# Optimization experiments

Measured on AMD Instinct MI355X. Metric: run time of the kernel, lower is better.

## Reference

```python
import jax, jax.numpy as jnp
import numpy as np
import math

DIM = 1024
NUM_HEADS = 16
HEAD_DIM = DIM // NUM_HEADS
BLOCK_SIZE = 64


def _block_mask(src_blocks, tgt_blocks, num_blocks):
    # Block-level BigBird mask: global first/last block columns, sliding window of 1, random blocks.
    i = jnp.arange(num_blocks)[:, None]
    j = jnp.arange(num_blocks)[None, :]
    band = jnp.abs(i - j) <= 1
    glob = (j == 0) | (j == num_blocks - 1)
    bm = band | glob
    bm = bm.at[src_blocks, tgt_blocks].set(True)
    return bm  # [nb, nb] bool


def setup_inputs() -> dict:
    key = jax.random.key(0)
    ks = jax.random.split(key, 12)
    B, S = 2, 2048
    x = jax.random.normal(ks[0], (B, S, DIM), dtype=jnp.float32)
    scale = 0.02
    Wq = jax.random.normal(ks[1], (DIM, DIM), dtype=jnp.float32) * scale
    bq = jnp.zeros((DIM,), dtype=jnp.float32)
    Wk = jax.random.normal(ks[2], (DIM, DIM), dtype=jnp.float32) * scale
    bk = jnp.zeros((DIM,), dtype=jnp.float32)
    Wv = jax.random.normal(ks[3], (DIM, DIM), dtype=jnp.float32) * scale
    bv = jnp.zeros((DIM,), dtype=jnp.float32)
    Wo = jax.random.normal(ks[4], (DIM, DIM), dtype=jnp.float32) * scale
    bo = jnp.zeros((DIM,), dtype=jnp.float32)
    num_blocks = S // BLOCK_SIZE
    src_blocks = jax.random.randint(ks[5], (3,), 0, num_blocks, dtype=jnp.int32)
    tgt_blocks = jax.random.randint(ks[6], (3,), 0, num_blocks, dtype=jnp.int32)
    return {"x": x, "Wq": Wq, "bq": bq, "Wk": Wk, "bk": bk, "Wv": Wv, "bv": bv,
            "Wo": Wo, "bo": bo, "src_blocks": src_blocks, "tgt_blocks": tgt_blocks}


def reference(x, Wq, bq, Wk, bk, Wv, bv, Wo, bo, src_blocks, tgt_blocks):
    B, S, _ = x.shape
    nb = S // BLOCK_SIZE
    # NOTE: original torch code uses .view (not transpose) to split heads; replicate faithfully.
    q = (x @ Wq.T + bq).reshape(B, NUM_HEADS, S, HEAD_DIM)
    k = (x @ Wk.T + bk).reshape(B, NUM_HEADS, S, HEAD_DIM)
    v = (x @ Wv.T + bv).reshape(B, NUM_HEADS, S, HEAD_DIM)
    bm = _block_mask(src_blocks, tgt_blocks, nb)
    mask = jnp.repeat(jnp.repeat(bm, BLOCK_SIZE, axis=0), BLOCK_SIZE, axis=1)  # [S, S]
    scores = jnp.einsum('bhqd,bhkd->bhqk', q, k) / math.sqrt(HEAD_DIM)
    scores = jnp.where(mask[None, None], scores, jnp.float32(-1e9))
    attn = jax.nn.softmax(scores, axis=-1)
    out = jnp.einsum('bhqk,bhkd->bhqd', attn, v)
    out = out.transpose(0, 2, 1, 3).reshape(B, S, DIM)
    return out @ Wo.T + bo
```

## Files before the change

### kernel.cpp

```cpp
#include <hip/hip_runtime.h>
#include <math.h>

typedef __attribute__((ext_vector_type(8))) short short8;
typedef __attribute__((ext_vector_type(4))) float f32x4;

#define SEQ 2048
#define NB  32

__device__ __forceinline__ unsigned short f2bf(float f) {
    unsigned u = __float_as_uint(f);
    u = (u + 0x7FFFu + ((u >> 16) & 1u)) >> 16;
    return (unsigned short)u;
}

__device__ __forceinline__ void gload16(const unsigned short* g, unsigned short* l) {
    __builtin_amdgcn_global_load_lds(
        (__attribute__((address_space(1))) void*)(void*)(g),
        (__attribute__((address_space(3))) void*)(l), 16, 0, 0);
}

__global__ __launch_bounds__(256) void cvt_all(const float* __restrict__ x,
                                               const float* __restrict__ w0,
                                               const float* __restrict__ w1,
                                               const float* __restrict__ w2,
                                               const float* __restrict__ w3,
                                               unsigned short* __restrict__ ox,
                                               unsigned short* __restrict__ o0,
                                               unsigned short* __restrict__ o1,
                                               unsigned short* __restrict__ o2,
                                               unsigned short* __restrict__ o3) {
    const int which = blockIdx.y;
    const float* in = (which == 0) ? x : (which == 1) ? w0 : (which == 2) ? w1
                       : (which == 3) ? w2 : w3;
    unsigned short* out = (which == 0) ? ox : (which == 1) ? o0 : (which == 2) ? o1
                          : (which == 3) ? o2 : o3;
    const int n8 = (which == 0) ? 524288 : 131072;
    int i = blockIdx.x * 256 + threadIdx.x;
    const int stride = gridDim.x * 256;
    for (; i < n8; i += stride) {
        const float4 a = ((const float4*)in)[i * 2];
        const float4 b = ((const float4*)in)[i * 2 + 1];
        uint4 o;
        o.x = f2bf(a.x) | ((unsigned)f2bf(a.y) << 16);
        o.y = f2bf(a.z) | ((unsigned)f2bf(a.w) << 16);
        o.z = f2bf(b.x) | ((unsigned)f2bf(b.y) << 16);
        o.w = f2bf(b.z) | ((unsigned)f2bf(b.w) << 16);
        ((uint4*)out)[i] = o;
    }
}

template <int BF16OUT, int BN>
__global__ __launch_bounds__(256) void gemm_bt(const unsigned short* __restrict__ A,
                                               const unsigned short* __restrict__ Wall,
                                               const float* __restrict__ b0,
                                               const float* __restrict__ b1,
                                               const float* __restrict__ b2,
                                               unsigned short* __restrict__ outb,
                                               float* __restrict__ outf) {
    constexpr int MI = (BN == 128) ? 4 : 2;
    constexpr int NI = 4;
    __shared__ __align__(16) unsigned short SMEM[2 * 128 * 32 + 2 * BN * 32];
    unsigned short* As0 = SMEM;
    unsigned short* As1 = SMEM + 128 * 32;
    unsigned short* Bs0 = SMEM + 2 * 128 * 32;
    unsigned short* Bs1 = SMEM + 2 * 128 * 32 + BN * 32;

    const int t = threadIdx.x;
    const int w = t >> 6, l = t & 63;
    const int bx = blockIdx.x;
    const int which = (BN == 128) ? (bx >> 3) : 0;
    const int n0 = (BN == 128) ? (bx & 7) * 128 : bx * 64;
    const int m0 = blockIdx.y * 128;
    const unsigned short* W = Wall + (size_t)which * (1024ull * 1024);
    const float* bias = (which == 0) ? b0 : (which == 1) ? b1 : b2;

    const int wr = (BN == 128) ? (w >> 1) * 64 : w * 32;
    const int wc = (BN == 128) ? (w & 1) * 64 : 0;

    f32x4 acc[MI][NI];
#pragma unroll
    for (int i = 0; i < MI; ++i)
#pragma unroll
        for (int j = 0; j < NI; ++j) acc[i][j] = f32x4{0.f, 0.f, 0.f, 0.f};

    const unsigned short* Ag = A + (size_t)(m0 + w * 32 + (l >> 2)) * 1024 + (l & 3) * 8;
    const unsigned short* Wg =
        W + (size_t)(n0 + ((BN == 128) ? w * 32 : w * 16) + (l >> 2)) * 1024 + (l & 3) * 8;

    auto STAGE = [&](unsigned short* Asb, unsigned short* Bsb, int k0) {
        gload16(Ag + k0, Asb + w * 1024);
        gload16(Ag + k0 + 16 * 1024, Asb + w * 1024 + 512);
        gload16(Wg + k0, Bsb + ((BN == 128) ? w * 1024 : w * 512));
        if (BN == 128) gload16(Wg + k0 + 16 * 1024, Bsb + w * 1024 + 512);
    };
    auto COMPUTE = [&](const unsigned short* Asb, const unsigned short* Bsb) {
        short8 af[MI], bfr[NI];
#pragma unroll
        for (int mi = 0; mi < MI; ++mi)
            af[mi] = *(const short8*)&Asb[(wr + mi * 16 + (l & 15)) * 32 + (l >> 4) * 8];
#pragma unroll
        for (int ni = 0; ni < NI; ++ni)
            bfr[ni] = *(const short8*)&Bsb[(wc + ni * 16 + (l & 15)) * 32 + (l >> 4) * 8];
#pragma unroll
        for (int mi = 0; mi < MI; ++mi)
#pragma unroll
            for (int ni = 0; ni < NI; ++ni)
                acc[mi][ni] = __builtin_amdgcn_mfma_f32_16x16x32_bf16(af[mi], bfr[ni],
                                                                      acc[mi][ni], 0, 0, 0);
    };
#define WAITV_INFLIGHT()                                                  \
    do {                                                                  \
        if constexpr (BN == 128)                                          \
            asm volatile("s_waitcnt vmcnt(4)" ::: "memory");              \
        else                                                              \
            asm volatile("s_waitcnt vmcnt(3)" ::: "memory");              \
        __builtin_amdgcn_sched_barrier(0);                                \
    } while (0)
#define BAR()                                                             \
    do {                                                                  \
        __builtin_amdgcn_s_barrier();                                     \
        __builtin_amdgcn_sched_barrier(0);                                \
    } while (0)
#define READS_DONE_BAR()                                                  \
    do {                                                                  \
        asm volatile("s_waitcnt lgkmcnt(0)" ::: "memory");                \
        __builtin_amdgcn_sched_barrier(0);                                \
        __builtin_amdgcn_s_barrier();                                     \
        __builtin_amdgcn_sched_barrier(0);                                \
    } while (0)

    STAGE(As0, Bs0, 0);
#pragma unroll 1
    for (int kt2 = 0; kt2 < 16; ++kt2) {
        STAGE(As1, Bs1, (kt2 * 2 + 1) * 32);
        WAITV_INFLIGHT();
        BAR();
        COMPUTE(As0, Bs0);
        READS_DONE_BAR();

        if (kt2 < 15) {
            STAGE(As0, Bs0, (kt2 * 2 + 2) * 32);
            WAITV_INFLIGHT();
        } else {
            asm volatile("s_waitcnt vmcnt(0)" ::: "memory");
            __builtin_amdgcn_sched_barrier(0);
        }
        BAR();
        COMPUTE(As1, Bs1);
        if (kt2 < 15) READS_DONE_BAR();
    }
#undef WAITV_INFLIGHT
#undef BAR
#undef READS_DONE_BAR

    __syncthreads();
    const int g = l >> 4, c = l & 15;
    if constexpr (BF16OUT) {
        unsigned short* eb = SMEM + w * (32 * 72);
        unsigned short* outw = outb + (size_t)which * (4096ull * 1024);
        const int r1 = l >> 1, hh = (l & 1) * 32;
#pragma unroll
        for (int half = 0; half < 2; ++half) {
#pragma unroll
            for (int ni = 0; ni < NI; ++ni) {
                const float bv = bias[n0 + wc + ni * 16 + c];
#pragma unroll
                for (int mi2 = 0; mi2 < 2; ++mi2)
#pragma unroll
                    for (int j = 0; j < 4; ++j)
                        eb[(mi2 * 16 + g * 4 + j) * 72 + ni * 16 + c] =
                            f2bf(acc[half * 2 + mi2][ni][j] + bv);
            }
            asm volatile("s_waitcnt lgkmcnt(0)" ::: "memory");
            __builtin_amdgcn_sched_barrier(0);
            const unsigned short* src = eb + r1 * 72 + hh;
            unsigned short* dst =
                &outw[(size_t)(m0 + wr + half * 32 + r1) * 1024 + n0 + wc + hh];
#pragma unroll
            for (int q = 0; q < 4; ++q)
                *(uint4*)(dst + q * 8) = *(const uint4*)(src + q * 8);
            asm volatile("s_waitcnt lgkmcnt(0)" ::: "memory");
            __builtin_amdgcn_sched_barrier(0);
        }
    } else {
        float* ef = (float*)SMEM + w * (16 * 68);
        const int r2 = l >> 2, qq = (l & 3) * 16;
#pragma unroll
        for (int mi = 0; mi < MI; ++mi) {
#pragma unroll
            for (int ni = 0; ni < NI; ++ni) {
                const float bv = bias[n0 + wc + ni * 16 + c];
#pragma unroll
                for (int j = 0; j < 4; ++j)
                    ef[(g * 4 + j) * 68 + ni * 16 + c] = acc[mi][ni][j] + bv;
            }
            asm volatile("s_waitcnt lgkmcnt(0)" ::: "memory");
            __builtin_amdgcn_sched_barrier(0);
            const float* srcf = ef + r2 * 68 + qq;
            float* dstf = &outf[(size_t)(m0 + wr + mi * 16 + r2) * 1024 + n0 + wc + qq];
#pragma unroll
            for (int q = 0; q < 4; ++q)
                *(float4*)(dstf + q * 4) = *(const float4*)(srcf + q * 4);
            asm volatile("s_waitcnt lgkmcnt(0)" ::: "memory");
            __builtin_amdgcn_sched_barrier(0);
        }
    }
}

__global__ __launch_bounds__(256) void gemm_obt(const unsigned short* __restrict__ A,
                                                const unsigned short* __restrict__ W,
                                                const float* __restrict__ bias,
                                                float* __restrict__ outf) {
    constexpr int MI = 2, NI = 4;
    __shared__ __align__(16) unsigned short SMEM[2 * (128 + 64) * 64];
    unsigned short* As0 = SMEM;
    unsigned short* As1 = SMEM + 128 * 64;
    unsigned short* Bs0 = SMEM + 2 * 128 * 64;
    unsigned short* Bs1 = SMEM + 2 * 128 * 64 + 64 * 64;

    const int t = threadIdx.x;
    const int w = t >> 6, l = t & 63;
    const int n0 = blockIdx.x * 64;
    const int m0 = blockIdx.y * 128;

    const int wr = w * 32, wc = 0;

    f32x4 acc[MI][NI];
#pragma unroll
    for (int i = 0; i < MI; ++i)
#pragma unroll
        for (int j = 0; j < NI; ++j) acc[i][j] = f32x4{0.f, 0.f, 0.f, 0.f};

    const int scol = ((l & 7) ^ (l >> 3)) * 8;
    const unsigned short* Ag = A + (size_t)(m0 + w * 32 + (l >> 3)) * 1024 + scol;
    const unsigned short* Wg = W + (size_t)(n0 + w * 16 + (l >> 3)) * 1024 + scol;

    auto STAGE = [&](unsigned short* Asb, unsigned short* Bsb, int k0) {
        gload16(Ag + k0, Asb + (w * 32) * 64);
        gload16(Ag + k0 + 8 * 1024, Asb + (w * 32 + 8) * 64);
        gload16(Ag + k0 + 16 * 1024, Asb + (w * 32 + 16) * 64);
        gload16(Ag + k0 + 24 * 1024, Asb + (w * 32 + 24) * 64);
        gload16(Wg + k0, Bsb + (w * 16) * 64);
        gload16(Wg + k0 + 8 * 1024, Bsb + (w * 16 + 8) * 64);
    };
    auto COMPUTE = [&](const unsigned short* Asb, const unsigned short* Bsb) {
#pragma unroll
        for (int kk = 0; kk < 2; ++kk) {
            short8 af[MI], bfr[NI];
#pragma unroll
            for (int mi = 0; mi < MI; ++mi) {
                const int r = wr + mi * 16 + (l & 15);
                const int slot = (kk * 4 + (l >> 4)) ^ (r & 7);
                af[mi] = *(const short8*)&Asb[r * 64 + slot * 8];
            }
#pragma unroll
            for (int ni = 0; ni < NI; ++ni) {
                const int r = wc + ni * 16 + (l & 15);
                const int slot = (kk * 4 + (l >> 4)) ^ (r & 7);
                bfr[ni] = *(const short8*)&Bsb[r * 64 + slot * 8];
            }
#pragma unroll
            for (int mi = 0; mi < MI; ++mi)
#pragma unroll
                for (int ni = 0; ni < NI; ++ni)
                    acc[mi][ni] = __builtin_amdgcn_mfma_f32_16x16x32_bf16(
                        af[mi], bfr[ni], acc[mi][ni], 0, 0, 0);
        }
    };
#define WV6()                                                             \
    do {                                                                  \
        asm volatile("s_waitcnt vmcnt(6)" ::: "memory");                  \
        __builtin_amdgcn_sched_barrier(0);                                \
    } while (0)
#define BAR()                                                             \
    do {                                                                  \
        __builtin_amdgcn_s_barrier();                                     \
        __builtin_amdgcn_sched_barrier(0);                                \
    } while (0)
#define READS_DONE_BAR()                                                  \
    do {                                                                  \
        asm volatile("s_waitcnt lgkmcnt(0)" ::: "memory");                \
        __builtin_amdgcn_sched_barrier(0);                                \
        __builtin_amdgcn_s_barrier();                                     \
        __builtin_amdgcn_sched_barrier(0);                                \
    } while (0)

    STAGE(As0, Bs0, 0);
#pragma unroll 1
    for (int kt2 = 0; kt2 < 8; ++kt2) {
        STAGE(As1, Bs1, (kt2 * 2 + 1) * 64);
        WV6();
        BAR();
        COMPUTE(As0, Bs0);
        READS_DONE_BAR();

        if (kt2 < 7) {
            STAGE(As0, Bs0, (kt2 * 2 + 2) * 64);
            WV6();
        } else {
            asm volatile("s_waitcnt vmcnt(0)" ::: "memory");
            __builtin_amdgcn_sched_barrier(0);
        }
        BAR();
        COMPUTE(As1, Bs1);
        if (kt2 < 7) READS_DONE_BAR();
    }
#undef WV6
#undef BAR
#undef READS_DONE_BAR

    __syncthreads();
    const int g = l >> 4, c = l & 15;
    float* ef = (float*)SMEM + w * (16 * 68);
    const int r2 = l >> 2, qq = (l & 3) * 16;
#pragma unroll
    for (int mi = 0; mi < MI; ++mi) {
#pragma unroll
        for (int ni = 0; ni < NI; ++ni) {
            const float bv = bias[n0 + wc + ni * 16 + c];
#pragma unroll
            for (int j = 0; j < 4; ++j)
                ef[(g * 4 + j) * 68 + ni * 16 + c] = acc[mi][ni][j] + bv;
        }
        asm volatile("s_waitcnt lgkmcnt(0)" ::: "memory");
        __builtin_amdgcn_sched_barrier(0);
        const float* srcf = ef + r2 * 68 + qq;
        float* dstf = &outf[(size_t)(m0 + wr + mi * 16 + r2) * 1024 + n0 + wc + qq];
#pragma unroll
        for (int q = 0; q < 4; ++q)
            *(float4*)(dstf + q * 4) = *(const float4*)(srcf + q * 4);
        asm volatile("s_waitcnt lgkmcnt(0)" ::: "memory");
        __builtin_amdgcn_sched_barrier(0);
    }
}

__global__ __launch_bounds__(256) void attn_mfma(const unsigned short* __restrict__ qb_,
                                                 const unsigned short* __restrict__ kb_,
                                                 const unsigned short* __restrict__ vb_,
                                                 const int* __restrict__ srcb,
                                                 const int* __restrict__ tgtb,
                                                 unsigned short* __restrict__ outb) {
    __shared__ __align__(16) unsigned short Ks[64 * 72];
    __shared__ __align__(16) unsigned short Vs[64 * 72];
    __shared__ __align__(16) unsigned short Ps[4][16 * 72];

    const int t = threadIdx.x, w = t >> 6, l = t & 63;
    const int qi = blockIdx.x, h = blockIdx.y, b = blockIdx.z;
    const int g = l >> 4, c = l & 15;

    unsigned mask = 1u | (1u << (NB - 1)) | (1u << qi);
    if (qi > 0) mask |= 1u << (qi - 1);
    if (qi < NB - 1) mask |= 1u << (qi + 1);
#pragma unroll
    for (int tt = 0; tt < 3; ++tt)
        if (srcb[tt] == qi) mask |= 1u << (tgtb[tt] & 31);

    const size_t ho = (size_t)(b * 16 + h) * (SEQ * 64);
    const unsigned short* Q = qb_ + ho;
    const unsigned short* K = kb_ + ho;
    const unsigned short* V = vb_ + ho;

    short8 qf[2];
    {
        const unsigned short* qrow = Q + (size_t)(qi * 64 + w * 16 + c) * 64;
        qf[0] = *(const short8*)(qrow + g * 8);
        qf[1] = *(const short8*)(qrow + 32 + g * 8);
    }

    f32x4 oacc[4];
#pragma unroll
    for (int d = 0; d < 4; ++d) oacc[d] = f32x4{0.f, 0.f, 0.f, 0.f};
    float mrun = -INFINITY, lsum = 0.f;

    const int sr = t >> 2, sc = (t & 3) * 16;

    uint4 k0, k1, v0, v1;
    {
        const unsigned short* ksrc = K + (size_t)(0 * 64 + sr) * 64 + sc;
        const unsigned short* vsrc = V + (size_t)(0 * 64 + sr) * 64 + sc;
        k0 = *(const uint4*)ksrc; k1 = *(const uint4*)(ksrc + 8);
        v0 = *(const uint4*)vsrc; v1 = *(const uint4*)(vsrc + 8);
    }

    int kb = 0;
    while (kb < NB) {
        int nxt = kb + 1;
        while (nxt < NB && !((mask >> nxt) & 1u)) ++nxt;

        __syncthreads();
        *(uint4*)&Ks[sr * 72 + sc] = k0;
        *(uint4*)&Ks[sr * 72 + sc + 8] = k1;
        {
            const unsigned short* p0 = (const unsigned short*)&v0;
            const unsigned short* p1 = (const unsigned short*)&v1;
#pragma unroll
            for (int e = 0; e < 8; ++e) {
                Vs[(sc + e) * 72 + sr] = p0[e];
                Vs[(sc + 8 + e) * 72 + sr] = p1[e];
            }
        }
        __syncthreads();

        if (nxt < NB) {
            const unsigned short* ksrc = K + (size_t)(nxt * 64 + sr) * 64 + sc;
            const unsigned short* vsrc = V + (size_t)(nxt * 64 + sr) * 64 + sc;
            k0 = *(const uint4*)ksrc; k1 = *(const uint4*)(ksrc + 8);
            v0 = *(const uint4*)vsrc; v1 = *(const uint4*)(vsrc + 8);
        }

        f32x4 sacc[4];
#pragma unroll
        for (int kt = 0; kt < 4; ++kt) sacc[kt] = f32x4{0.f, 0.f, 0.f, 0.f};
#pragma unroll
        for (int kt = 0; kt < 4; ++kt) {
#pragma unroll
            for (int ks = 0; ks < 2; ++ks) {
                const short8 ka = *(const short8*)&Ks[(kt * 16 + c) * 72 + ks * 32 + g * 8];
                sacc[kt] = __builtin_amdgcn_mfma_f32_16x16x32_bf16(ka, qf[ks], sacc[kt], 0, 0, 0);
            }
        }

        float sv[16];
        float tmax = -INFINITY;
#pragma unroll
        for (int kt = 0; kt < 4; ++kt)
#pragma unroll
            for (int j = 0; j < 4; ++j) {
                const float x = sacc[kt][j] * 0.125f;
                sv[kt * 4 + j] = x;
                tmax = fmaxf(tmax, x);
            }
        tmax = fmaxf(tmax, __shfl_xor(tmax, 16));
        tmax = fmaxf(tmax, __shfl_xor(tmax, 32));
        const float newm = fmaxf(mrun, tmax);
        const float corr = __expf(mrun - newm);
        float ps = 0.f;
#pragma unroll
        for (int e = 0; e < 16; ++e) {
            const float p = __expf(sv[e] - newm);
            sv[e] = p;
            ps += p;
        }
        ps += __shfl_xor(ps, 16);
        ps += __shfl_xor(ps, 32);
        lsum = lsum * corr + ps;
        mrun = newm;
#pragma unroll
        for (int d = 0; d < 4; ++d)
#pragma unroll
            for (int j = 0; j < 4; ++j) oacc[d][j] *= corr;

        unsigned short* pw = &Ps[w][c * 72];
#pragma unroll
        for (int kt = 0; kt < 4; ++kt) {
            uint2 pk;
            pk.x = f2bf(sv[kt * 4 + 0]) | ((unsigned)f2bf(sv[kt * 4 + 1]) << 16);
            pk.y = f2bf(sv[kt * 4 + 2]) | ((unsigned)f2bf(sv[kt * 4 + 3]) << 16);
            *(uint2*)&pw[kt * 16 + g * 4] = pk;
        }
        asm volatile("s_waitcnt lgkmcnt(0)" ::: "memory");
        __builtin_amdgcn_sched_barrier(0);

#pragma unroll
        for (int ks = 0; ks < 2; ++ks) {
            const short8 pb = *(const short8*)&Ps[w][c * 72 + ks * 32 + g * 8];
#pragma unroll
            for (int dt = 0; dt < 4; ++dt) {
                const short8 va = *(const short8*)&Vs[(dt * 16 + c) * 72 + ks * 32 + g * 8];
                oacc[dt] = __builtin_amdgcn_mfma_f32_16x16x32_bf16(va, pb, oacc[dt], 0, 0, 0);
            }
        }

        kb = nxt;
    }

    const float inv = 1.f / lsum;
    unsigned short* orow = outb + (size_t)(b * SEQ + qi * 64 + w * 16 + c) * 1024 + h * 64;
#pragma unroll
    for (int dt = 0; dt < 4; ++dt)
#pragma unroll
        for (int j = 0; j < 4; ++j)
            orow[dt * 16 + g * 4 + j] = f2bf(oacc[dt][j] * inv);
}

extern "C" void kernel_launch(void* const* d_in, const int* in_sizes, int n_in,
                              void* d_out, int out_size, void* d_ws, size_t ws_size,
                              hipStream_t stream) {
    const float* x  = (const float*)d_in[0];
    const float* Wq = (const float*)d_in[1];
    const float* bq = (const float*)d_in[2];
    const float* Wk = (const float*)d_in[3];
    const float* bk = (const float*)d_in[4];
    const float* Wv = (const float*)d_in[5];
    const float* bv = (const float*)d_in[6];
    const float* Wo = (const float*)d_in[7];
    const float* bo = (const float*)d_in[8];
    const int* srcb = (const int*)d_in[9];
    const int* tgtb = (const int*)d_in[10];

    unsigned short* wsu = (unsigned short*)d_ws;
    unsigned short* xbf   = wsu;
    unsigned short* wqkv  = wsu + 4194304ull;
    unsigned short* wobf  = wsu + 7340032ull;
    unsigned short* qkvbf = wsu + 8388608ull;
    unsigned short* attbf = wsu + 25165824ull;

    hipLaunchKernelGGL(cvt_all, dim3(512, 5), dim3(256), 0, stream,
                       x, Wq, Wk, Wv, Wo,
                       xbf, wqkv, wqkv + 1048576ull, wqkv + 2097152ull, wobf);

    hipLaunchKernelGGL((gemm_bt<1, 128>), dim3(24, 32), dim3(256), 0, stream,
                       xbf, wqkv, bq, bk, bv, qkvbf, (float*)nullptr);

    hipLaunchKernelGGL(attn_mfma, dim3(32, 16, 2), dim3(256), 0, stream,
                       qkvbf, qkvbf + 4194304ull, qkvbf + 2ull * 4194304ull,
                       srcb, tgtb, attbf);

    hipLaunchKernelGGL(gemm_obt, dim3(16, 32), dim3(256), 0, stream,
                       attbf, wobf, bo, (float*)d_out);

    (void)in_sizes; (void)n_in; (void)out_size; (void)ws_size;
}
```

Before: 92.30 us.

## Split-K the output projection GEMM with atomic accumulation

Splits the K dimension of the output projection GEMM into two halves across blockIdx.z, doubling the grid from 512 to 1024 blocks. Partial results are combined with float atomicAdd into the output, which is zeroed by a memset beforehand, and only the first split adds the bias. The aim is better CU occupancy for this small GEMM. In exchange it adds scattered uncoalesced atomic traffic, an extra memset, and non-deterministic summation order.

```diff
diff --git a/kernel.cpp b/kernel.cpp
--- a/kernel.cpp
+++ b/kernel.cpp
@@ -207,10 +207,10 @@
     }
 }
 
-__global__ __launch_bounds__(256) void gemm_obt(const unsigned short* __restrict__ A,
-                                                const unsigned short* __restrict__ W,
-                                                const float* __restrict__ bias,
-                                                float* __restrict__ outf) {
+__global__ __launch_bounds__(256) void gemm_obt_sk(const unsigned short* __restrict__ A,
+                                                   const unsigned short* __restrict__ W,
+                                                   const float* __restrict__ bias,
+                                                   float* __restrict__ outf) {
     constexpr int MI = 2, NI = 4;
     __shared__ __align__(16) unsigned short SMEM[2 * (128 + 64) * 64];
     unsigned short* As0 = SMEM;
@@ -222,6 +222,8 @@
     const int w = t >> 6, l = t & 63;
     const int n0 = blockIdx.x * 64;
     const int m0 = blockIdx.y * 128;
+    const int kz = blockIdx.z;
+    const int kbase = kz * 512;
 
     const int wr = w * 32, wc = 0;
 
@@ -285,17 +287,17 @@
         __builtin_amdgcn_sched_barrier(0);                                \
     } while (0)
 
-    STAGE(As0, Bs0, 0);
+    STAGE(As0, Bs0, kbase);
 #pragma unroll 1
-    for (int kt2 = 0; kt2 < 8; ++kt2) {
-        STAGE(As1, Bs1, (kt2 * 2 + 1) * 64);
+    for (int kt2 = 0; kt2 < 4; ++kt2) {
+        STAGE(As1, Bs1, kbase + (kt2 * 2 + 1) * 64);
         WV6();
         BAR();
         COMPUTE(As0, Bs0);
         READS_DONE_BAR();
 
-        if (kt2 < 7) {
-            STAGE(As0, Bs0, (kt2 * 2 + 2) * 64);
+        if (kt2 < 3) {
+            STAGE(As0, Bs0, kbase + (kt2 * 2 + 2) * 64);
             WV6();
         } else {
             asm volatile("s_waitcnt vmcnt(0)" ::: "memory");
@@ -303,34 +305,24 @@
         }
         BAR();
         COMPUTE(As1, Bs1);
-        if (kt2 < 7) READS_DONE_BAR();
+        if (kt2 < 3) READS_DONE_BAR();
     }
 #undef WV6
 #undef BAR
 #undef READS_DONE_BAR
 
-    __syncthreads();
     const int g = l >> 4, c = l & 15;
-    float* ef = (float*)SMEM + w * (16 * 68);
-    const int r2 = l >> 2, qq = (l & 3) * 16;
-#pragma unroll
-    for (int mi = 0; mi < MI; ++mi) {
-#pragma unroll
-        for (int ni = 0; ni < NI; ++ni) {
-            const float bv = bias[n0 + wc + ni * 16 + c];
-#pragma unroll
-            for (int j = 0; j < 4; ++j)
-                ef[(g * 4 + j) * 68 + ni * 16 + c] = acc[mi][ni][j] + bv;
-        }
-        asm volatile("s_waitcnt lgkmcnt(0)" ::: "memory");
-        __builtin_amdgcn_sched_barrier(0);
-        const float* srcf = ef + r2 * 68 + qq;
-        float* dstf = &outf[(size_t)(m0 + wr + mi * 16 + r2) * 1024 + n0 + wc + qq];
-#pragma unroll
-        for (int q = 0; q < 4; ++q)
-            *(float4*)(dstf + q * 4) = *(const float4*)(srcf + q * 4);
-        asm volatile("s_waitcnt lgkmcnt(0)" ::: "memory");
-        __builtin_amdgcn_sched_barrier(0);
+#pragma unroll
+    for (int ni = 0; ni < NI; ++ni) {
+        const int n = n0 + wc + ni * 16 + c;
+        const float bv = (kz == 0) ? bias[n] : 0.f;
+#pragma unroll
+        for (int mi = 0; mi < MI; ++mi)
+#pragma unroll
+            for (int j = 0; j < 4; ++j) {
+                const size_t m = (size_t)(m0 + wr + mi * 16 + g * 4 + j);
+                atomicAdd(&outf[m * 1024 + n], acc[mi][ni][j] + bv);
+            }
     }
 }
 
@@ -505,6 +497,8 @@
     unsigned short* qkvbf = wsu + 8388608ull;
     unsigned short* attbf = wsu + 25165824ull;
 
+    hipMemsetAsync(d_out, 0, (size_t)out_size * sizeof(float), stream);
+
     hipLaunchKernelGGL(cvt_all, dim3(512, 5), dim3(256), 0, stream,
                        x, Wq, Wk, Wv, Wo,
                        xbf, wqkv, wqkv + 1048576ull, wqkv + 2097152ull, wobf);
@@ -516,7 +510,7 @@
                        qkvbf, qkvbf + 4194304ull, qkvbf + 2ull * 4194304ull,
                        srcb, tgtb, attbf);
 
-    hipLaunchKernelGGL(gemm_obt, dim3(16, 32), dim3(256), 0, stream,
+    hipLaunchKernelGGL(gemm_obt_sk, dim3(16, 32, 2), dim3(256), 0, stream,
                        attbf, wobf, bo, (float*)d_out);
 
     (void)in_sizes; (void)n_in; (void)out_size; (void)ws_size;
```

Result: slower. 111.7 us (+21.0%).
